# Optimization experiments

Measured on AMD Instinct MI355X. Metric: run time of the kernel, lower is better.

Reference implementation:

```python
import jax, jax.numpy as jnp
import numpy as np
from jax import lax

VOCAB = 18
EMB = 200
HID = 200
SEQ = 128
BATCH = 2048
PAD_IDX = 0


def setup_inputs() -> dict:
    key = jax.random.key(0)
    ks = jax.random.split(key, 8)
    s_emb = 1.0  # torch nn.Embedding default N(0,1)
    s_lstm = 1.0 / np.sqrt(HID)  # torch LSTM default U(-1/sqrt(H), 1/sqrt(H))
    s_lin = 1.0 / np.sqrt(HID)
    inp = {
        "x": jax.random.randint(ks[0], (BATCH, SEQ), 0, VOCAB, dtype=jnp.int32),
        "E": jax.random.normal(ks[1], (VOCAB, EMB), dtype=jnp.float32) * s_emb,
        "W_ih": jax.random.uniform(ks[2], (4 * HID, EMB), minval=-s_lstm, maxval=s_lstm, dtype=jnp.float32),
        "W_hh": jax.random.uniform(ks[3], (4 * HID, HID), minval=-s_lstm, maxval=s_lstm, dtype=jnp.float32),
        "b_ih": jax.random.uniform(ks[4], (4 * HID,), minval=-s_lstm, maxval=s_lstm, dtype=jnp.float32),
        "b_hh": jax.random.uniform(ks[5], (4 * HID,), minval=-s_lstm, maxval=s_lstm, dtype=jnp.float32),
        "W_out": jax.random.uniform(ks[6], (VOCAB, HID), minval=-s_lin, maxval=s_lin, dtype=jnp.float32),
        "b_out": jax.random.uniform(ks[7], (VOCAB,), minval=-s_lin, maxval=s_lin, dtype=jnp.float32),
    }
    return inp


def _forward(x, E, W_ih, W_hh, b_ih, b_hh, W_out, b_out):
    # Embedding with padding_idx=0 (row 0 is zero, no grad flows to it)
    pad_mask = (jnp.arange(VOCAB) != PAD_IDX).astype(E.dtype)[:, None]
    emb = (E * pad_mask)[x]  # (B, T, EMB)
    B = emb.shape[0]
    # Precompute input contribution to all gates for every timestep
    x_proj = jnp.einsum("bte,ge->btg", emb, W_ih) + b_ih + b_hh  # (B, T, 4H)

    def step(carry, xg_t):
        h, c = carry
        gates = xg_t + h @ W_hh.T  # (B, 4H)
        i, f, g, o = jnp.split(gates, 4, axis=-1)  # torch gate order i,f,g,o
        i = jax.nn.sigmoid(i)
        f = jax.nn.sigmoid(f)
        g = jnp.tanh(g)
        o = jax.nn.sigmoid(o)
        c = f * c + i * g
        h = o * jnp.tanh(c)
        return (h, c), h

    h0 = jnp.zeros((B, HID), dtype=emb.dtype)
    c0 = jnp.zeros((B, HID), dtype=emb.dtype)
    (h_n, c_n), hs = lax.scan(step, (h0, c0), x_proj.transpose(1, 0, 2))
    out = hs.transpose(1, 0, 2)  # (B, T, HID)
    logits = out @ W_out.T + b_out  # (B, T, VOCAB)
    return logits, h_n, c_n


def reference(x, E, W_ih, W_hh, b_ih, b_hh, W_out, b_out):
    return _forward(x, E, W_ih, W_hh, b_ih, b_hh, W_out, b_out)
```

## Files before the change

kernel.cpp:

```cpp
#include <hip/hip_runtime.h>

#define VOCAB 18
#define EMB   200
#define HID   200
#define G4    800
#define SEQ   128
#define BATCH 2048
#define MB    8
#define NT    56
#define KS    7
#define TPB   256
#define TPW   14
#define SV    (SEQ*VOCAB)
#define LOGITS_N ((size_t)BATCH*SEQ*VOCAB)

typedef short s16x8 __attribute__((ext_vector_type(8)));
typedef float f32x4 __attribute__((ext_vector_type(4)));

__device__ __forceinline__ unsigned short f2bf(float f) {
  unsigned int u = __float_as_uint(f);
  u += 0x7FFFu + ((u >> 16) & 1u);
  return (unsigned short)(u >> 16);
}
__device__ __forceinline__ float sigm(float x) {
  float e = __builtin_amdgcn_exp2f(x * 1.4426950408889634f);
  return e * __builtin_amdgcn_rcpf(e + 1.0f);
}
__device__ __forceinline__ float tanhq(float x) {
  float e = __builtin_amdgcn_exp2f(x * 2.8853900817779268f);
  return 1.0f - 2.0f * __builtin_amdgcn_rcpf(e + 1.0f);
}
__device__ __forceinline__ float dpp_x1(float v) {
  return __uint_as_float((unsigned)__builtin_amdgcn_mov_dpp(
      (int)__float_as_uint(v), 0xB1, 0xF, 0xF, true));
}
__device__ __forceinline__ float dpp_x2(float v) {
  return __uint_as_float((unsigned)__builtin_amdgcn_mov_dpp(
      (int)__float_as_uint(v), 0x4E, 0xF, 0xF, true));
}

__global__ void prep_tbl(const float* __restrict__ E, const float* __restrict__ W_ih,
                         const float* __restrict__ b_ih, const float* __restrict__ b_hh,
                         unsigned short* __restrict__ tbl) {
  int tid = blockIdx.x * 256 + threadIdx.x;
  if (tid >= VOCAB * G4) return;
  int v = tid / G4, col = tid % G4;
  float s = b_ih[col] + b_hh[col];
  if (v != 0) {
    const float* Er = E + v * EMB;
    const float* Wr = W_ih + col * EMB;
    for (int e = 0; e < EMB; ++e) s += Er[e] * Wr[e];
  }
  tbl[tid] = f2bf(s);
}

__global__ void prep_wp(const float* __restrict__ W_hh, const float* __restrict__ W_out,
                        const float* __restrict__ b_out,
                        const unsigned short* __restrict__ tbl,
                        short* __restrict__ Wp) {
  int u = blockIdx.x * 256 + threadIdx.x;
  if (u >= NT * KS * 64) return;
  int n    = u / (KS * 64);
  int rem  = u % (KS * 64);
  int s_   = rem >> 6;
  int lane = rem & 63;
  int c    = lane & 15;
  int kb   = lane >> 4;
  s16x8 o;
  #pragma unroll
  for (int i = 0; i < 8; ++i) {
    int k = 32 * s_ + 8 * kb + i;
    short b = 0;
    if (n < 50) {
      int g = c & 3, j = 4 * n + (c >> 2);
      int colg = g * 200 + j;
      if (k < HID)                          b = (short)f2bf(W_hh[colg * HID + k]);
      else if (k >= 201 && k < 201 + VOCAB) b = (short)tbl[(k - 201) * G4 + colg];
    } else if (n < 52) {
      int v = 16 * (n - 50) + c;
      if (v < VOCAB) {
        if (k < HID)       b = (short)f2bf(W_out[v * HID + k]);
        else if (k == HID) b = (short)f2bf(b_out[v]);
      }
    }
    o[i] = b;
  }
  *(s16x8*)(Wp + (size_t)u * 8) = o;
}

__global__ __launch_bounds__(TPB) __attribute__((amdgpu_waves_per_eu(1, 1)))
void lstm_kernel(const int* __restrict__ x, const short* __restrict__ Wp,
                 float* __restrict__ out) {
  __shared__ unsigned short hA[KS * 64 * 8];
  __shared__ int   xtok[MB * SEQ];
  __shared__ float logL[MB * SV];

  const int tid  = threadIdx.x;
  const int lane = tid & 63;
  const int w    = tid >> 6;
  const int blk  = blockIdx.x;
  const int jw   = 56 * w;
  const int jj   = (lane >> 2) & 3;
  const int row  = 4 * ((lane >> 4) & 3) + (lane & 3);
  const bool pb0 = lane & 1, pb1 = lane & 2;

  for (int i = tid; i < KS * 64 * 8; i += TPB)
    hA[i] = (i >= 3200 && i < 3264 && (i & 7) == 0) ? (unsigned short)0x3F80
                                                    : (unsigned short)0;
  for (int i = tid; i < MB * SEQ; i += TPB) xtok[i] = x[blk * (MB * SEQ) + i];

  s16x8 wf[TPW][KS];
  #pragma unroll
  for (int n = 0; n < TPW; ++n) {
    #pragma unroll
    for (int s = 0; s < KS; ++s) {
      wf[n][s] = *(const s16x8*)(Wp + ((((w * TPW + n) * KS) + s) * 64 + lane) * 8);
      asm volatile("" : "+a"(wf[n][s]));
    }
    asm volatile("" ::: "memory");
  }

  float cA[7] = {0,0,0,0,0,0,0}, cB[7] = {0,0,0,0,0,0,0};
  const f32x4 zz = {0.f, 0.f, 0.f, 0.f};
  __syncthreads();

#define MFMA_PAIR(nt, A, B) {                                                   \
    _Pragma("unroll")                                                           \
    for (int s = 0; s < KS; ++s) {                                              \
      A = __builtin_amdgcn_mfma_f32_16x16x32_bf16(aF[s], wf[nt][s],     A, 0,0,0); \
      B = __builtin_amdgcn_mfma_f32_16x16x32_bf16(aF[s], wf[(nt)+1][s], B, 0,0,0); \
    } }

#define TRANS4(v) {                                                             \
    float t0 = dpp_x1(v[0]), t1 = dpp_x1(v[1]), t2 = dpp_x1(v[2]), t3 = dpp_x1(v[3]); \
    v[0] = pb0 ? t1 : v[0];  v[1] = pb0 ? v[1] : t0;                            \
    v[2] = pb0 ? t3 : v[2];  v[3] = pb0 ? v[3] : t2;                            \
    t0 = dpp_x2(v[0]); t1 = dpp_x2(v[1]); t2 = dpp_x2(v[2]); t3 = dpp_x2(v[3]); \
    v[0] = pb1 ? t2 : v[0];  v[1] = pb1 ? t3 : v[1];                            \
    v[2] = pb1 ? v[2] : t0;  v[3] = pb1 ? v[3] : t1; }

#define EWONE(V, CC, J) {                                                       \
    float i_ = sigm(V[0]), f_ = sigm(V[1]), g_ = tanhq(V[2]), o_ = sigm(V[3]);  \
    float cn = f_ * (CC) + i_ * g_;                                             \
    float h  = o_ * tanhq(cn);                                                  \
    (CC) = cn;                                                                  \
    hA[(((J) >> 5) * 64 + 16 * (((J) >> 3) & 3) + row) * 8 + ((J) & 7)] = f2bf(h); \
    if (t == SEQ - 1) {                                                         \
      size_t bg = (size_t)blk * MB + row;                                       \
      out[LOGITS_N + bg * HID + (J)] = h;                                       \
      out[LOGITS_N + (size_t)BATCH * HID + bg * HID + (J)] = cn;                \
    } }

#define EW_PAIR(P, A, B) {                                                      \
    TRANS4(A); TRANS4(B);                                                       \
    if (lane < 32) {                                                            \
      int jA = jw + 8 * (P) + jj;                                               \
      EWONE(A, cA[P], jA);                                                      \
      EWONE(B, cB[P], jA + 4);                                                  \
    } }

#define LOGIT_STORE(A, B)                                                       \
    if (t > 0 && lane < 32) {                                                   \
      int qrow = (lane >> 4) * 4, c = lane & 15;                                \
      _Pragma("unroll")                                                         \
      for (int q = 0; q < 4; ++q) {                                             \
        logL[(qrow + q) * SV + (t - 1) * VOCAB + c] = A[q];                     \
        if (c < 2) logL[(qrow + q) * SV + (t - 1) * VOCAB + 16 + c] = B[q];     \
      } }

  #pragma unroll 1
  for (int t = 0; t < SEQ; ++t) {
    s16x8 aF[KS];
    #pragma unroll
    for (int s = 0; s < KS; ++s) aF[s] = *(const s16x8*)&hA[(s * 64 + lane) * 8];
    {
      int vv = xtok[(lane & 7) * SEQ + t];
      int js = (lane & 8) ? 100 : (vv + 9 - 8 * (lane >> 4));
      s16x8 a6 = aF[6];
      #pragma unroll
      for (int e = 0; e < 8; ++e)
        a6[e] = (e == js) ? (short)0x3F80 : a6[e];
      aF[6] = a6;
    }
    __syncthreads();

    if (w < 3) {
      f32x4 A0 = zz, B0 = zz, A1 = zz, B1 = zz;
      MFMA_PAIR(0, A0, B0);
      MFMA_PAIR(2, A1, B1);   EW_PAIR(0, A0, B0);
      A0 = zz; B0 = zz;
      MFMA_PAIR(4, A0, B0);   EW_PAIR(1, A1, B1);
      A1 = zz; B1 = zz;
      MFMA_PAIR(6, A1, B1);   EW_PAIR(2, A0, B0);
      A0 = zz; B0 = zz;
      MFMA_PAIR(8, A0, B0);   EW_PAIR(3, A1, B1);
      A1 = zz; B1 = zz;
      MFMA_PAIR(10, A1, B1);  EW_PAIR(4, A0, B0);
      A0 = zz; B0 = zz;
      MFMA_PAIR(12, A0, B0);  EW_PAIR(5, A1, B1);
      EW_PAIR(6, A0, B0);
    } else {
      f32x4 A0 = zz, B0 = zz, A1 = zz, B1 = zz;
      MFMA_PAIR(0, A0, B0);
      MFMA_PAIR(2, A1, B1);   EW_PAIR(0, A0, B0);
      A0 = zz; B0 = zz;
      MFMA_PAIR(4, A0, B0);   EW_PAIR(1, A1, B1);
      A1 = zz; B1 = zz;
      MFMA_PAIR(6, A1, B1);   EW_PAIR(2, A0, B0);
      A0 = zz; B0 = zz;
      MFMA_PAIR(8, A0, B0);   EW_PAIR(3, A1, B1);
      LOGIT_STORE(A0, B0);
    }
    __syncthreads();
  }

  if (w == 3) {
    s16x8 aF[KS];
    #pragma unroll
    for (int s = 0; s < KS; ++s) aF[s] = *(const s16x8*)&hA[(s * 64 + lane) * 8];
    f32x4 A0 = zz, B0 = zz;
    MFMA_PAIR(8, A0, B0);
    if (lane < 32) {
      int qrow = (lane >> 4) * 4, c = lane & 15;
      #pragma unroll
      for (int q = 0; q < 4; ++q) {
        int base = (qrow + q) * SV + (SEQ - 1) * VOCAB;
        logL[base + c] = A0[q];
        if (c < 2) logL[base + 16 + c] = B0[q];
      }
    }
  }
  __syncthreads();

  float* dst = out + (size_t)blk * (MB * SV);
  for (int i = tid * 4; i < MB * SV; i += TPB * 4)
    *(f32x4*)&dst[i] = *(const f32x4*)&logL[i];

#undef MFMA_PAIR
#undef TRANS4
#undef EWONE
#undef EW_PAIR
#undef LOGIT_STORE
}

extern "C" void kernel_launch(void* const* d_in, const int* in_sizes, int n_in,
                              void* d_out, int out_size, void* d_ws, size_t ws_size,
                              hipStream_t stream) {
  const int*   x     = (const int*)  d_in[0];
  const float* E     = (const float*)d_in[1];
  const float* W_ih  = (const float*)d_in[2];
  const float* W_hh  = (const float*)d_in[3];
  const float* b_ih  = (const float*)d_in[4];
  const float* b_hh  = (const float*)d_in[5];
  const float* W_out = (const float*)d_in[6];
  const float* b_out = (const float*)d_in[7];
  float* out = (float*)d_out;

  unsigned short* tbl = (unsigned short*)d_ws;
  short* Wp = (short*)d_ws + VOCAB * G4;

  prep_tbl<<<(VOCAB * G4 + 255) / 256, 256, 0, stream>>>(E, W_ih, b_ih, b_hh, tbl);
  prep_wp<<<(NT * KS * 64 + 255) / 256, 256, 0, stream>>>(W_hh, W_out, b_out, tbl, Wp);
  lstm_kernel<<<BATCH / MB, TPB, 0, stream>>>(x, Wp, out);
}
```

Baseline: 426.4 us.

## Swap MFMA operand order to drop DPP transposes and write one-hot into shared memory

Weights now go in as the A operand and hidden state as B, so each lane's accumulator already holds the four gates of one hidden unit for one batch row. That removes the two-stage DPP transpose before the elementwise LSTM update. The per-step token one-hot is no longer patched into registers after the LDS load. Eight threads instead clear the previous token's entry and set the next one directly in the shared hidden buffer before the barrier. The risk is a slightly different lane-to-output mapping for the gate update and logit stores, plus extra LDS writes each step.

```diff
diff --git a/kernel.cpp b/kernel.cpp
--- a/kernel.cpp
+++ b/kernel.cpp
@@ -30,13 +30,9 @@
   float e = __builtin_amdgcn_exp2f(x * 2.8853900817779268f);
   return 1.0f - 2.0f * __builtin_amdgcn_rcpf(e + 1.0f);
 }
-__device__ __forceinline__ float dpp_x1(float v) {
-  return __uint_as_float((unsigned)__builtin_amdgcn_mov_dpp(
-      (int)__float_as_uint(v), 0xB1, 0xF, 0xF, true));
-}
-__device__ __forceinline__ float dpp_x2(float v) {
-  return __uint_as_float((unsigned)__builtin_amdgcn_mov_dpp(
-      (int)__float_as_uint(v), 0x4E, 0xF, 0xF, true));
+
+__device__ __forceinline__ int oh_elem(int c, int k) {
+  return (384 + ((k >> 3) & 3) * 16 + c) * 8 + (k & 7);
 }
 
 __global__ void prep_tbl(const float* __restrict__ E, const float* __restrict__ W_ih,
@@ -64,7 +60,7 @@
   int rem  = u % (KS * 64);
   int s_   = rem >> 6;
   int lane = rem & 63;
-  int c    = lane & 15;
+  int rr   = lane & 15;
   int kb   = lane >> 4;
   s16x8 o;
   #pragma unroll
@@ -72,12 +68,12 @@
     int k = 32 * s_ + 8 * kb + i;
     short b = 0;
     if (n < 50) {
-      int g = c & 3, j = 4 * n + (c >> 2);
+      int g = rr & 3, j = 4 * n + (rr >> 2);
       int colg = g * 200 + j;
       if (k < HID)                          b = (short)f2bf(W_hh[colg * HID + k]);
       else if (k >= 201 && k < 201 + VOCAB) b = (short)tbl[(k - 201) * G4 + colg];
     } else if (n < 52) {
-      int v = 16 * (n - 50) + c;
+      int v = 16 * (n - 50) + rr;
       if (v < VOCAB) {
         if (k < HID)       b = (short)f2bf(W_out[v * HID + k]);
         else if (k == HID) b = (short)f2bf(b_out[v]);
@@ -100,9 +96,9 @@
   const int w    = tid >> 6;
   const int blk  = blockIdx.x;
   const int jw   = 56 * w;
-  const int jj   = (lane >> 2) & 3;
-  const int row  = 4 * ((lane >> 4) & 3) + (lane & 3);
-  const bool pb0 = lane & 1, pb1 = lane & 2;
+  const bool hi8 = lane & 8;
+  const int c8   = lane & 7;
+  const int kb   = lane >> 4;
 
   for (int i = tid; i < KS * 64 * 8; i += TPB)
     hA[i] = (i >= 3200 && i < 3264 && (i & 7) == 0) ? (unsigned short)0x3F80
@@ -120,52 +116,47 @@
     asm volatile("" ::: "memory");
   }
 
-  float cA[7] = {0,0,0,0,0,0,0}, cB[7] = {0,0,0,0,0,0,0};
+  __syncthreads();
+  if (tid < MB) hA[oh_elem(tid, 201 + xtok[tid * SEQ])] = 0x3F80;
+
+  float ccA[7] = {0, 0, 0, 0, 0, 0, 0};
+  float ccB[7] = {0, 0, 0, 0, 0, 0, 0};
   const f32x4 zz = {0.f, 0.f, 0.f, 0.f};
   __syncthreads();
 
 #define MFMA_PAIR(nt, A, B) {                                                   \
     _Pragma("unroll")                                                           \
     for (int s = 0; s < KS; ++s) {                                              \
-      A = __builtin_amdgcn_mfma_f32_16x16x32_bf16(aF[s], wf[nt][s],     A, 0,0,0); \
-      B = __builtin_amdgcn_mfma_f32_16x16x32_bf16(aF[s], wf[(nt)+1][s], B, 0,0,0); \
+      A = __builtin_amdgcn_mfma_f32_16x16x32_bf16(wf[nt][s],     aF[s], A, 0,0,0); \
+      B = __builtin_amdgcn_mfma_f32_16x16x32_bf16(wf[(nt)+1][s], aF[s], B, 0,0,0); \
     } }
 
-#define TRANS4(v) {                                                             \
-    float t0 = dpp_x1(v[0]), t1 = dpp_x1(v[1]), t2 = dpp_x1(v[2]), t3 = dpp_x1(v[3]); \
-    v[0] = pb0 ? t1 : v[0];  v[1] = pb0 ? v[1] : t0;                            \
-    v[2] = pb0 ? t3 : v[2];  v[3] = pb0 ? v[3] : t2;                            \
-    t0 = dpp_x2(v[0]); t1 = dpp_x2(v[1]); t2 = dpp_x2(v[2]); t3 = dpp_x2(v[3]); \
-    v[0] = pb1 ? t2 : v[0];  v[1] = pb1 ? t3 : v[1];                            \
-    v[2] = pb1 ? v[2] : t0;  v[3] = pb1 ? v[3] : t1; }
-
-#define EWONE(V, CC, J) {                                                       \
+#define EW_ONE(V, CC, J) {                                                      \
     float i_ = sigm(V[0]), f_ = sigm(V[1]), g_ = tanhq(V[2]), o_ = sigm(V[3]);  \
     float cn = f_ * (CC) + i_ * g_;                                             \
     float h  = o_ * tanhq(cn);                                                  \
     (CC) = cn;                                                                  \
-    hA[(((J) >> 5) * 64 + 16 * (((J) >> 3) & 3) + row) * 8 + ((J) & 7)] = f2bf(h); \
+    hA[(((J) >> 5) * 64 + 16 * (((J) >> 3) & 3) + c8) * 8 + ((J) & 7)] = f2bf(h); \
     if (t == SEQ - 1) {                                                         \
-      size_t bg = (size_t)blk * MB + row;                                       \
+      size_t bg = (size_t)blk * MB + c8;                                        \
       out[LOGITS_N + bg * HID + (J)] = h;                                       \
       out[LOGITS_N + (size_t)BATCH * HID + bg * HID + (J)] = cn;                \
     } }
 
-#define EW_PAIR(P, A, B) {                                                      \
-    TRANS4(A); TRANS4(B);                                                       \
-    if (lane < 32) {                                                            \
-      int jA = jw + 8 * (P) + jj;                                               \
-      EWONE(A, cA[P], jA);                                                      \
-      EWONE(B, cB[P], jA + 4);                                                  \
-    } }
-
-#define LOGIT_STORE(A, B)                                                       \
-    if (t > 0 && lane < 32) {                                                   \
-      int qrow = (lane >> 4) * 4, c = lane & 15;                                \
+#define EW_PAIR(P, A, B)                                                        \
+    if (!hi8) {                                                                 \
+      int J0 = jw + 8 * (P) + kb;                                               \
+      EW_ONE(A, ccA[P], J0);                                                    \
+      EW_ONE(B, ccB[P], J0 + 4);                                                \
+    }
+
+#define LOGIT_STORE(TT, A, B)                                                   \
+    if (!hi8) {                                                                 \
+      int vg = 4 * kb;                                                          \
       _Pragma("unroll")                                                         \
       for (int q = 0; q < 4; ++q) {                                             \
-        logL[(qrow + q) * SV + (t - 1) * VOCAB + c] = A[q];                     \
-        if (c < 2) logL[(qrow + q) * SV + (t - 1) * VOCAB + 16 + c] = B[q];     \
+        logL[c8 * SV + (TT) * VOCAB + vg + q] = A[q];                           \
+        if (vg + q < 2) logL[c8 * SV + (TT) * VOCAB + 16 + vg + q] = B[q];      \
       } }
 
   #pragma unroll 1
@@ -173,15 +164,6 @@
     s16x8 aF[KS];
     #pragma unroll
     for (int s = 0; s < KS; ++s) aF[s] = *(const s16x8*)&hA[(s * 64 + lane) * 8];
-    {
-      int vv = xtok[(lane & 7) * SEQ + t];
-      int js = (lane & 8) ? 100 : (vv + 9 - 8 * (lane >> 4));
-      s16x8 a6 = aF[6];
-      #pragma unroll
-      for (int e = 0; e < 8; ++e)
-        a6[e] = (e == js) ? (short)0x3F80 : a6[e];
-      aF[6] = a6;
-    }
     __syncthreads();
 
     if (w < 3) {
@@ -209,7 +191,13 @@
       MFMA_PAIR(6, A1, B1);   EW_PAIR(2, A0, B0);
       A0 = zz; B0 = zz;
       MFMA_PAIR(8, A0, B0);   EW_PAIR(3, A1, B1);
-      LOGIT_STORE(A0, B0);
+      if (t > 0) LOGIT_STORE(t - 1, A0, B0);
+    }
+    if (tid < MB && t + 1 < SEQ) {
+      int v0 = xtok[tid * SEQ + t];
+      int v1 = xtok[tid * SEQ + t + 1];
+      hA[oh_elem(tid, 201 + v0)] = 0;
+      hA[oh_elem(tid, 201 + v1)] = 0x3F80;
     }
     __syncthreads();
   }
@@ -220,15 +208,7 @@
     for (int s = 0; s < KS; ++s) aF[s] = *(const s16x8*)&hA[(s * 64 + lane) * 8];
     f32x4 A0 = zz, B0 = zz;
     MFMA_PAIR(8, A0, B0);
-    if (lane < 32) {
-      int qrow = (lane >> 4) * 4, c = lane & 15;
-      #pragma unroll
-      for (int q = 0; q < 4; ++q) {
-        int base = (qrow + q) * SV + (SEQ - 1) * VOCAB;
-        logL[base + c] = A0[q];
-        if (c < 2) logL[base + 16 + c] = B0[q];
-      }
-    }
+    LOGIT_STORE(SEQ - 1, A0, B0);
   }
   __syncthreads();
 
@@ -237,8 +217,7 @@
     *(f32x4*)&dst[i] = *(const f32x4*)&logL[i];
 
 #undef MFMA_PAIR
-#undef TRANS4
-#undef EWONE
+#undef EW_ONE
 #undef EW_PAIR
 #undef LOGIT_STORE
 }
```

Result: no change. 432.3 us (+1.4%).
